# Kernel tuning notes

Measured on AMD Instinct MI355X. Metric: run time of the kernel, lower is better.

The kernel has to match this reference:

```python
import jax, jax.numpy as jnp
import numpy as np


def setup_inputs() -> dict:
    key = jax.random.key(0)
    k1, k2 = jax.random.split(key)
    inputs = jax.random.normal(k1, (4, 8, 24, 24, 64), dtype=jnp.float32)
    gamma = jax.random.normal(k2, (1,), dtype=jnp.float32)
    return {"inputs": inputs, "gamma": gamma}


def reference(inputs, gamma):
    # inputs: (B, D, H, W, C); flatten spatial dims to N = D*H*W
    B, D, H, W, C = inputs.shape
    N = D * H * W
    q = inputs.reshape(B, N, C)                       # proj_query (B, N, C)
    # energy = Q @ Q^T -> (B, N, N)
    energy = jnp.einsum('bnc,bmc->bnm', q, q)
    attention = jax.nn.softmax(energy, axis=-1)       # softmax over last axis
    out = jnp.einsum('bnm,bmc->bnc', attention, q)    # (B, N, C)
    out = out.reshape(B, D, H, W, C)
    return gamma * out + inputs
```

## Files before the change

### kernel.cpp

```cpp
#include <hip/hip_runtime.h>

typedef __bf16 bf16_t;
typedef bf16_t bf16x8 __attribute__((ext_vector_type(8)));
typedef float  f32x4  __attribute__((ext_vector_type(4)));
typedef unsigned int u32;
typedef unsigned short u16;

#define B_SZ   4
#define N_SZ   4608
#define C_SZ   64
#define KVB    32
#define QROWS  32
#define NKVT   (N_SZ / KVB)
#define NQT    (N_SZ / QROWS)
#define WV     4
#define TPW    (NKVT / WV)

__device__ __forceinline__ f32x4 mfma16(bf16x8 a, bf16x8 b, f32x4 c) {
  return __builtin_amdgcn_mfma_f32_16x16x32_bf16(a, b, c, 0, 0, 0);
}

__device__ __forceinline__ u32 pk2(float a, float b) {
  u16 ua = __builtin_bit_cast(u16, (bf16_t)a);
  u16 ub = __builtin_bit_cast(u16, (bf16_t)b);
  return (u32)ua | ((u32)ub << 16);
}

__global__ __launch_bounds__(256) void transform_k(
    const float* __restrict__ in, bf16_t* __restrict__ khi,
    bf16_t* __restrict__ klo, bf16_t* __restrict__ vt) {
  __shared__ float tile[64 * 65];
  const int bid = blockIdx.x;
  const int b  = bid / 72;
  const int n0 = (bid - b * 72) * 64;
  const int t  = threadIdx.x;
  {
    const int nl = t >> 2, c0 = (t & 3) * 16;
    const float* src = in + ((size_t)(b * N_SZ + n0 + nl)) * C_SZ + c0;
    float v[16];
    *(float4*)(v +  0) = *(const float4*)(src +  0);
    *(float4*)(v +  4) = *(const float4*)(src +  4);
    *(float4*)(v +  8) = *(const float4*)(src +  8);
    *(float4*)(v + 12) = *(const float4*)(src + 12);
    bf16x8 h8[2], l8[2];
#pragma unroll
    for (int i = 0; i < 16; ++i) {
      bf16_t h = (bf16_t)v[i];
      h8[i >> 3][i & 7] = h;
      l8[i >> 3][i & 7] = (bf16_t)(v[i] - (float)h);
      tile[nl * 65 + c0 + i] = v[i];
    }
    bf16_t* dh = khi + ((size_t)(b * N_SZ + n0 + nl)) * C_SZ + c0;
    bf16_t* dl = klo + ((size_t)(b * N_SZ + n0 + nl)) * C_SZ + c0;
    *(bf16x8*)(dh) = h8[0]; *(bf16x8*)(dh + 8) = h8[1];
    *(bf16x8*)(dl) = l8[0]; *(bf16x8*)(dl + 8) = l8[1];
  }
  __syncthreads();
  {
    const int c = t >> 2, m0 = (t & 3) * 16;
    bf16x8 o[2];
#pragma unroll
    for (int i = 0; i < 16; ++i)
      o[i >> 3][i & 7] = (bf16_t)tile[(m0 + i) * 65 + c];
    bf16_t* dst = vt + ((size_t)(b * C_SZ + c)) * N_SZ + n0 + m0;
    *(bf16x8*)(dst) = o[0]; *(bf16x8*)(dst + 8) = o[1];
  }
}

__global__ __launch_bounds__(256, 3) void attn_fwd(
    const float* __restrict__ in, const bf16_t* __restrict__ khi,
    const bf16_t* __restrict__ klo, const bf16_t* __restrict__ vt,
    const float* __restrict__ gamma_p, float* __restrict__ out) {
  __shared__ float obuf[256 * 36];
  __shared__ float mlbuf[4 * 2 * 2 * 16];

  const int bid0 = blockIdx.x;
  const int bid  = (bid0 & 7) * 72 + (bid0 >> 3);
  const int b  = bid / NQT;
  const int qt = bid - b * NQT;
  const int t  = threadIdx.x;
  const int w  = t >> 6, l = t & 63;
  const int c15 = l & 15, g = l >> 4;

  const bf16_t* kh_b = khi + (size_t)b * N_SZ * C_SZ;
  const bf16_t* kl_b = klo + (size_t)b * N_SZ * C_SZ;
  const bf16_t* vt_b = vt  + (size_t)b * C_SZ * N_SZ;

  bf16x8 qh[2][2], ql[2][2];
#pragma unroll
  for (int j = 0; j < 2; ++j)
#pragma unroll
    for (int ks = 0; ks < 2; ++ks) {
      const size_t a = (size_t)(qt * QROWS + j * 16 + c15) * C_SZ + ks * 32 + g * 8;
      qh[j][ks] = *(const bf16x8*)(kh_b + a);
      ql[j][ks] = *(const bf16x8*)(kl_b + a);
    }

  f32x4 acc[4][2];
#pragma unroll
  for (int co = 0; co < 4; ++co)
#pragma unroll
    for (int j = 0; j < 2; ++j)
      acc[co][j] = (f32x4){0.f, 0.f, 0.f, 0.f};
  float m_j[2] = {-3.0e38f, -3.0e38f}, l_j[2] = {0.f, 0.f};

  const int sA = ((l >> 4) & 1) * 32 + c15;
  const int sB = sA + 16;
  const bool hi_half = (l >= 32);

  for (int it = 0; it < TPW; ++it) {
    const int kv0 = (w + it * WV) * KVB;

    bf16x8 khf[2][2], klf[2][2];
#pragma unroll
    for (int ct = 0; ct < 2; ++ct)
#pragma unroll
      for (int ks = 0; ks < 2; ++ks) {
        const size_t a = (size_t)(kv0 + ct * 16 + c15) * C_SZ + ks * 32 + g * 8;
        khf[ct][ks] = *(const bf16x8*)(kh_b + a);
        klf[ct][ks] = *(const bf16x8*)(kl_b + a);
      }
    bf16x8 vf[4];
#pragma unroll
    for (int co = 0; co < 4; ++co)
      vf[co] = *(const bf16x8*)(vt_b + (size_t)(co * 16 + c15) * N_SZ + kv0 + g * 8);

    f32x4 s[2][2];
#pragma unroll
    for (int j = 0; j < 2; ++j)
#pragma unroll
      for (int ct = 0; ct < 2; ++ct) {
        f32x4 a = (f32x4){0.f, 0.f, 0.f, 0.f};
#pragma unroll
        for (int ks = 0; ks < 2; ++ks) {
          a = mfma16(khf[ct][ks], qh[j][ks], a);
          a = mfma16(khf[ct][ks], ql[j][ks], a);
          a = mfma16(klf[ct][ks], qh[j][ks], a);
        }
        s[j][ct] = a;
      }

#pragma unroll
    for (int j = 0; j < 2; ++j) {
      float mx = fmaxf(fmaxf(fmaxf(s[j][0][0], s[j][0][1]), fmaxf(s[j][0][2], s[j][0][3])),
                       fmaxf(fmaxf(s[j][1][0], s[j][1][1]), fmaxf(s[j][1][2], s[j][1][3])));
      mx = fmaxf(mx, __shfl_xor(mx, 16, 64));
      mx = fmaxf(mx, __shfl_xor(mx, 32, 64));
      const float mn = fmaxf(m_j[j], mx);
      const float sc = __expf(m_j[j] - mn);
      m_j[j] = mn;
      float rs = 0.f;
#pragma unroll
      for (int ct = 0; ct < 2; ++ct)
#pragma unroll
        for (int r = 0; r < 4; ++r) {
          const float e = __expf(s[j][ct][r] - mn);
          s[j][ct][r] = e;
          rs += e;
        }
      rs += __shfl_xor(rs, 16, 64);
      rs += __shfl_xor(rs, 32, 64);
      l_j[j] = l_j[j] * sc + rs;
#pragma unroll
      for (int co = 0; co < 4; ++co)
        acc[co][j] *= sc;

      const u32 L0 = pk2(s[j][0][0], s[j][0][1]);
      const u32 H0 = pk2(s[j][0][2], s[j][0][3]);
      const u32 L1 = pk2(s[j][1][0], s[j][1][1]);
      const u32 H1 = pk2(s[j][1][2], s[j][1][3]);
      const u32 aL0 = (u32)__shfl((int)L0, sA, 64);
      const u32 aL1 = (u32)__shfl((int)L1, sA, 64);
      const u32 aH0 = (u32)__shfl((int)H0, sA, 64);
      const u32 aH1 = (u32)__shfl((int)H1, sA, 64);
      const u32 bL0 = (u32)__shfl((int)L0, sB, 64);
      const u32 bL1 = (u32)__shfl((int)L1, sB, 64);
      const u32 bH0 = (u32)__shfl((int)H0, sB, 64);
      const u32 bH1 = (u32)__shfl((int)H1, sB, 64);
      union { u32 u[4]; bf16x8 v; } pf;
      pf.u[0] = hi_half ? aL1 : aL0;
      pf.u[1] = hi_half ? aH1 : aH0;
      pf.u[2] = hi_half ? bL1 : bL0;
      pf.u[3] = hi_half ? bH1 : bH0;
#pragma unroll
      for (int co = 0; co < 4; ++co)
        acc[co][j] = mfma16(vf[co], pf.v, acc[co][j]);
    }
  }

  float* ob = obuf + (size_t)(w * 64 + l) * 36;
#pragma unroll
  for (int co = 0; co < 4; ++co)
#pragma unroll
    for (int j = 0; j < 2; ++j)
      *(f32x4*)(ob + (co * 2 + j) * 4) = acc[co][j];
  if (g == 0) {
#pragma unroll
    for (int j = 0; j < 2; ++j) {
      mlbuf[((w * 2 + j) * 2 + 0) * 16 + c15] = m_j[j];
      mlbuf[((w * 2 + j) * 2 + 1) * 16 + c15] = l_j[j];
    }
  }
  __syncthreads();

  const float gm = gamma_p[0];
#pragma unroll
  for (int j = 0; j < 2; ++j) {
    float mw[4];
#pragma unroll
    for (int wp = 0; wp < 4; ++wp)
      mw[wp] = mlbuf[((wp * 2 + j) * 2 + 0) * 16 + c15];
    const float ms = fmaxf(fmaxf(mw[0], mw[1]), fmaxf(mw[2], mw[3]));
    float ls = 0.f;
    f32x4 mg = (f32x4){0.f, 0.f, 0.f, 0.f};
#pragma unroll
    for (int wp = 0; wp < 4; ++wp) {
      const float cf = __expf(mw[wp] - ms);
      ls += cf * mlbuf[((wp * 2 + j) * 2 + 1) * 16 + c15];
      const f32x4 pv = *(const f32x4*)(obuf + (size_t)(wp * 64 + l) * 36 + (w * 2 + j) * 4);
      mg += pv * cf;
    }
    const float inv = 1.0f / ls;
    const int q  = qt * QROWS + j * 16 + c15;
    const int cb = w * 16 + g * 4;
    const size_t base = ((size_t)(b * N_SZ + q)) * C_SZ + cb;
    const float4 iv = *(const float4*)(in + base);
    float4 ov;
    ov.x = gm * (mg[0] * inv) + iv.x;
    ov.y = gm * (mg[1] * inv) + iv.y;
    ov.z = gm * (mg[2] * inv) + iv.z;
    ov.w = gm * (mg[3] * inv) + iv.w;
    *(float4*)(out + base) = ov;
  }
}

extern "C" void kernel_launch(void* const* d_in, const int* in_sizes, int n_in,
                              void* d_out, int out_size, void* d_ws, size_t ws_size,
                              hipStream_t stream) {
  const float* in = (const float*)d_in[0];
  const float* gp = (const float*)d_in[1];
  float* op = (float*)d_out;
  const size_t plane = (size_t)B_SZ * N_SZ * C_SZ;
  bf16_t* khi = (bf16_t*)d_ws;
  bf16_t* klo = khi + plane;
  bf16_t* vt  = klo + plane;
  hipLaunchKernelGGL(transform_k, dim3(288), dim3(256), 0, stream, in, khi, klo, vt);
  hipLaunchKernelGGL(attn_fwd, dim3(B_SZ * NQT), dim3(256), 0, stream,
                     in, khi, klo, vt, gp, op);
}
```

Baseline: 208.8 us.

## Prefetch next KV tile into registers while computing current tile

Software-pipelines the attention loop: the K-hi, K-lo and V fragments for the next KV tile are loaded into a second register set before the current tile's MFMAs and softmax run, then swapped in at the end of the iteration. The aim is to hide global-memory latency behind compute. The added registers led to lowering launch bounds from 3 to 2 blocks per CU, which reduces occupancy. The P-fragment packing also moves from a union to a bit_cast vector, and the last iteration issues a wasted reload of tile 0.

```diff
diff --git a/kernel.cpp b/kernel.cpp
--- a/kernel.cpp
+++ b/kernel.cpp
@@ -4,6 +4,7 @@
 typedef bf16_t bf16x8 __attribute__((ext_vector_type(8)));
 typedef float  f32x4  __attribute__((ext_vector_type(4)));
 typedef unsigned int u32;
+typedef u32    u32x4  __attribute__((ext_vector_type(4)));
 typedef unsigned short u16;
 
 #define B_SZ   4
@@ -67,7 +68,22 @@
   }
 }
 
-__global__ __launch_bounds__(256, 3) void attn_fwd(
+#define LOAD_TILE(KV0, KH, KL, VF)                                             \
+  {                                                                            \
+    _Pragma("unroll")                                                          \
+    for (int ct = 0; ct < 2; ++ct)                                             \
+      _Pragma("unroll")                                                        \
+      for (int ks = 0; ks < 2; ++ks) {                                         \
+        const size_t a = (size_t)((KV0) + ct * 16 + c15) * C_SZ + ks * 32 + g * 8; \
+        KH[ct][ks] = *(const bf16x8*)(kh_b + a);                               \
+        KL[ct][ks] = *(const bf16x8*)(kl_b + a);                               \
+      }                                                                        \
+    _Pragma("unroll")                                                          \
+    for (int co = 0; co < 4; ++co)                                             \
+      VF[co] = *(const bf16x8*)(vt_b + (size_t)(co * 16 + c15) * N_SZ + (KV0) + g * 8); \
+  }
+
+__global__ __launch_bounds__(256, 2) void attn_fwd(
     const float* __restrict__ in, const bf16_t* __restrict__ khi,
     const bf16_t* __restrict__ klo, const bf16_t* __restrict__ vt,
     const float* __restrict__ gamma_p, float* __restrict__ out) {
@@ -108,22 +124,14 @@
   const int sB = sA + 16;
   const bool hi_half = (l >= 32);
 
+  bf16x8 khf[2][2], klf[2][2], vf[4];
+  LOAD_TILE(w * KVB, khf, klf, vf);
+
   for (int it = 0; it < TPW; ++it) {
-    const int kv0 = (w + it * WV) * KVB;
-
-    bf16x8 khf[2][2], klf[2][2];
-#pragma unroll
-    for (int ct = 0; ct < 2; ++ct)
-#pragma unroll
-      for (int ks = 0; ks < 2; ++ks) {
-        const size_t a = (size_t)(kv0 + ct * 16 + c15) * C_SZ + ks * 32 + g * 8;
-        khf[ct][ks] = *(const bf16x8*)(kh_b + a);
-        klf[ct][ks] = *(const bf16x8*)(kl_b + a);
-      }
-    bf16x8 vf[4];
-#pragma unroll
-    for (int co = 0; co < 4; ++co)
-      vf[co] = *(const bf16x8*)(vt_b + (size_t)(co * 16 + c15) * N_SZ + kv0 + g * 8);
+    const int itn = (it + 1 < TPW) ? it + 1 : 0;
+    const int kvn = (w + itn * WV) * KVB;
+    bf16x8 nkh[2][2], nkl[2][2], nvf[4];
+    LOAD_TILE(kvn, nkh, nkl, nvf);
 
     f32x4 s[2][2];
 #pragma unroll
@@ -177,15 +185,26 @@
       const u32 bL1 = (u32)__shfl((int)L1, sB, 64);
       const u32 bH0 = (u32)__shfl((int)H0, sB, 64);
       const u32 bH1 = (u32)__shfl((int)H1, sB, 64);
-      union { u32 u[4]; bf16x8 v; } pf;
-      pf.u[0] = hi_half ? aL1 : aL0;
-      pf.u[1] = hi_half ? aH1 : aH0;
-      pf.u[2] = hi_half ? bL1 : bL0;
-      pf.u[3] = hi_half ? bH1 : bH0;
+      const u32x4 pw = (u32x4){hi_half ? aL1 : aL0,
+                               hi_half ? aH1 : aH0,
+                               hi_half ? bL1 : bL0,
+                               hi_half ? bH1 : bH0};
+      const bf16x8 pfv = __builtin_bit_cast(bf16x8, pw);
 #pragma unroll
       for (int co = 0; co < 4; ++co)
-        acc[co][j] = mfma16(vf[co], pf.v, acc[co][j]);
-    }
+        acc[co][j] = mfma16(vf[co], pfv, acc[co][j]);
+    }
+
+#pragma unroll
+    for (int ct = 0; ct < 2; ++ct)
+#pragma unroll
+      for (int ks = 0; ks < 2; ++ks) {
+        khf[ct][ks] = nkh[ct][ks];
+        klf[ct][ks] = nkl[ct][ks];
+      }
+#pragma unroll
+    for (int co = 0; co < 4; ++co)
+      vf[co] = nvf[co];
   }
 
   float* ob = obuf + (size_t)(w * 64 + l) * 36;
```

After: 208.9 us. No clear change (+0.1%).
